# Optimization experiments

Measured on AMD Instinct MI355X. Metric: run time of the kernel, lower is better.

Reference implementation:

```python
import jax, jax.numpy as jnp
import numpy as np

D_MODEL = 1024
NUM_HEADS = 16
DEPTH = D_MODEL // NUM_HEADS
B, S = 2, 2048


def setup_inputs() -> dict:
    key = jax.random.key(0)
    ks = jax.random.split(key, 12)
    scale = 1.0 / np.sqrt(D_MODEL)
    inp = {
        "Q": jax.random.normal(ks[0], (B, S, D_MODEL), jnp.float32),
        "K": jax.random.normal(ks[1], (B, S, D_MODEL), jnp.float32),
        "V": jax.random.normal(ks[2], (B, S, D_MODEL), jnp.float32),
        # causal mask: 1 where attention is disallowed (strictly upper triangular)
        "mask": jnp.triu(jnp.ones((1, 1, S, S), jnp.float32), k=1),
        "Wq": jax.random.normal(ks[3], (D_MODEL, D_MODEL), jnp.float32) * scale,
        "bq": jnp.zeros((D_MODEL,), jnp.float32),
        "Wk": jax.random.normal(ks[4], (D_MODEL, D_MODEL), jnp.float32) * scale,
        "bk": jnp.zeros((D_MODEL,), jnp.float32),
        "Wv": jax.random.normal(ks[5], (D_MODEL, D_MODEL), jnp.float32) * scale,
        "bv": jnp.zeros((D_MODEL,), jnp.float32),
        "Wo": jax.random.normal(ks[6], (D_MODEL, D_MODEL), jnp.float32) * scale,
        "bo": jnp.zeros((D_MODEL,), jnp.float32),
    }
    return inp


def _split_heads(x):
    # [B, S, d_model] -> [B, H, S, depth]
    b, s, _ = x.shape
    return x.reshape(b, s, NUM_HEADS, DEPTH).transpose(0, 2, 1, 3)


def reference(Q, K, V, mask, Wq, bq, Wk, bk, Wv, bv, Wo, bo):
    q = _split_heads(Q @ Wq + bq)  # [B,H,S,depth]
    k = _split_heads(K @ Wk + bk)
    v = _split_heads(V @ Wv + bv)

    scale = 1.0 / jnp.sqrt(jnp.asarray(DEPTH, q.dtype))
    scores = jnp.einsum("bhqd,bhkd->bhqk", q, k) * scale
    scores = scores + mask * (-1e9)
    attn = jax.nn.softmax(scores, axis=-1)  # [B,H,S,S]
    ctx = jnp.einsum("bhqk,bhkd->bhqd", attn, v)

    # combine heads: [B,H,S,depth] -> [B,S,d_model]
    ctx = ctx.transpose(0, 2, 1, 3).reshape(Q.shape[0], -1, D_MODEL)
    out = ctx @ Wo + bo
    return out, attn
```

## Files before the change

kernel.cpp:

```cpp
#include <hip/hip_runtime.h>
#include <hip/hip_bf16.h>
#include <cstdint>
#include <cstddef>


typedef __bf16 bf16x8 __attribute__((ext_vector_type(8)));
typedef float  f32x4  __attribute__((ext_vector_type(4)));
typedef short  short8 __attribute__((ext_vector_type(8)));
typedef unsigned short u16;
typedef unsigned int   u32;

using gas_p = const __attribute__((address_space(1))) void*;
using las_p = __attribute__((address_space(3))) void*;

static __device__ __forceinline__ u16 f2bf(float x) {
    unsigned u = __builtin_bit_cast(unsigned, x);
    u += 0x7FFFu + ((u >> 16) & 1u);
    return (u16)(u >> 16);
}
static __device__ __forceinline__ u32 pk2(float a, float b) {
    return (u32)f2bf(a) | ((u32)f2bf(b) << 16);
}
static __device__ __forceinline__ f32x4 mfma16(bf16x8 a, bf16x8 b, f32x4 c) {
    return __builtin_amdgcn_mfma_f32_16x16x32_bf16(a, b, c, 0, 0, 0);
}
static __device__ __forceinline__ bf16x8 ldb8(const u16* p) {
    return *reinterpret_cast<const bf16x8*>(p);
}

__global__ __launch_bounds__(256) void cvt_bf16_k(const float* __restrict__ Q,
                                                  const float* __restrict__ K,
                                                  const float* __restrict__ V,
                                                  u16* __restrict__ Qb,
                                                  u16* __restrict__ Kb,
                                                  u16* __restrict__ Vb) {
    const int z = blockIdx.y;
    const float* in = (z == 0) ? Q : (z == 1) ? K : V;
    u16* out = (z == 0) ? Qb : (z == 1) ? Kb : Vb;
    size_t i = (size_t)blockIdx.x * 256 + threadIdx.x;
    const float4* p = reinterpret_cast<const float4*>(in) + 2 * i;
    float4 a = p[0], b = p[1];
    short8 r;
    r[0] = (short)f2bf(a.x); r[1] = (short)f2bf(a.y);
    r[2] = (short)f2bf(a.z); r[3] = (short)f2bf(a.w);
    r[4] = (short)f2bf(b.x); r[5] = (short)f2bf(b.y);
    r[6] = (short)f2bf(b.z); r[7] = (short)f2bf(b.w);
    *reinterpret_cast<short8*>(out + 8 * i) = r;
}

__global__ __launch_bounds__(256) void transpose_cvt_k(const float* __restrict__ Wq,
                                                       const float* __restrict__ Wk,
                                                       const float* __restrict__ Wv,
                                                       const float* __restrict__ Wo,
                                                       u16* __restrict__ Wt3,
                                                       u16* __restrict__ Wto) {
    const int z = blockIdx.z;
    const float* in = (z == 0) ? Wq : (z == 1) ? Wk : (z == 2) ? Wv : Wo;
    u16* out = (z < 3) ? (Wt3 + (size_t)z * 1048576) : Wto;
    __shared__ float t[32][33];
    const int tx = threadIdx.x, ty = threadIdx.y;
    const int x  = blockIdx.x * 32 + tx;
    const int y0 = blockIdx.y * 32 + ty;
#pragma unroll
    for (int j = 0; j < 32; j += 8)
        t[ty + j][tx] = in[(size_t)(y0 + j) * 1024 + x];
    __syncthreads();
    const int x2 = blockIdx.y * 32 + tx;
    const int y2 = blockIdx.x * 32 + ty;
#pragma unroll
    for (int j = 0; j < 32; j += 8)
        out[(size_t)(y2 + j) * 1024 + x2] = f2bf(t[tx][ty + j]);
}

__global__ __launch_bounds__(256) void gemm_qkv_k(const u16* __restrict__ Qb,
                                                  const u16* __restrict__ Kb,
                                                  const u16* __restrict__ Vb,
                                                  const u16* __restrict__ Wt3,
                                                  const float* __restrict__ bq,
                                                  const float* __restrict__ bk,
                                                  const float* __restrict__ bv,
                                                  u16* __restrict__ qf,
                                                  u16* __restrict__ kf,
                                                  u16* __restrict__ vtf,
                                                  float* __restrict__ attn) {
    constexpr int Kd = 1024;
    constexpr int S = 2048;
    const int z = blockIdx.z;

    if (z == 3) {
        float* attn_h = attn + (size_t)blockIdx.y * S * S;
        const int bx = blockIdx.x;
        const int ro = threadIdx.x >> 4, cc = threadIdx.x & 15;
        const f32x4 zz = {0.f, 0.f, 0.f, 0.f};
        for (int c = 1; c < 32; ++c) {
            float* base = attn_h + (size_t)(bx * 8 * c) * S + c * 64 + cc * 4;
            const int nrows = 8 * c;
            for (int i = ro; i < nrows; i += 16)
                *reinterpret_cast<f32x4*>(base + (size_t)i * S) = zz;
        }
        return;
    }

    const u16* A  = (z == 0) ? Qb : (z == 1) ? Kb : Vb;
    const u16* Bt = Wt3 + (size_t)z * 1048576;
    const float* bias = (z == 0) ? bq : (z == 1) ? bk : bv;

    __shared__ __align__(16) u16 As[128 * 64];
    __shared__ __align__(16) u16 Bs[128 * 64];
    const int tid = threadIdx.x;
    const int w = tid >> 6, lane = tid & 63;
    const int g = lane >> 4, lr = lane & 15;
    const int wr = w >> 1, wc = w & 1;
    const int bm = blockIdx.y * 128, bn = blockIdx.x * 128;

    f32x4 acc[4][4];
#pragma unroll
    for (int a = 0; a < 4; ++a)
#pragma unroll
        for (int b = 0; b < 4; ++b) acc[a][b] = f32x4{0.f, 0.f, 0.f, 0.f};

    for (int kt = 0; kt < Kd; kt += 64) {
#pragma unroll
        for (int it = 0; it < 4; ++it) {
            const int t2  = it * 256 + tid;
            const int row = t2 >> 3, ch = t2 & 7;
            const int ub  = (it * 256 + w * 64) * 8;
            __builtin_amdgcn_global_load_lds(
                (gas_p)(A + (size_t)(bm + row) * Kd + kt + ch * 8),
                (las_p)(As + ub), 16, 0, 0);
            __builtin_amdgcn_global_load_lds(
                (gas_p)(Bt + (size_t)(bn + row) * Kd + kt + ch * 8),
                (las_p)(Bs + ub), 16, 0, 0);
        }
        __syncthreads();
#pragma unroll
        for (int kk = 0; kk < 2; ++kk) {
            bf16x8 af[4], bfv[4];
#pragma unroll
            for (int mi = 0; mi < 4; ++mi)
                af[mi] = ldb8(As + (wr * 64 + mi * 16 + lr) * 64 + kk * 32 + g * 8);
#pragma unroll
            for (int ni = 0; ni < 4; ++ni)
                bfv[ni] = ldb8(Bs + (wc * 64 + ni * 16 + lr) * 64 + kk * 32 + g * 8);
#pragma unroll
            for (int mi = 0; mi < 4; ++mi)
#pragma unroll
                for (int ni = 0; ni < 4; ++ni)
                    acc[mi][ni] = mfma16(af[mi], bfv[ni], acc[mi][ni]);
        }
        __syncthreads();
    }

#pragma unroll
    for (int ni = 0; ni < 4; ++ni) {
        const int col = bn + wc * 64 + ni * 16 + lr;
        const float bvv = bias[col];
#pragma unroll
        for (int mi = 0; mi < 4; ++mi) {
            const int row0 = bm + wr * 64 + mi * 16 + g * 4;
            f32x4 c = acc[mi][ni];
            if (z == 2) {
                const int b = row0 >> 11, s0 = row0 & 2047;
                const int h = col >> 6,  d = col & 63;
                ushort4 pk;
                pk.x = f2bf(c[0] + bvv); pk.y = f2bf(c[1] + bvv);
                pk.z = f2bf(c[2] + bvv); pk.w = f2bf(c[3] + bvv);
                *reinterpret_cast<ushort4*>(
                    vtf + ((size_t)(b * 16 + h) * 64 + d) * 2048 + s0) = pk;
            } else {
#pragma unroll
                for (int i = 0; i < 4; ++i) {
                    const int row = row0 + i;
                    const int b = row >> 11, s = row & 2047;
                    const int h = col >> 6,  d = col & 63;
                    u16* dst = (z == 0) ? qf : kf;
                    dst[((size_t)(b * 16 + h) * 2048 + s) * 64 + d] =
                        f2bf(c[i] + bvv);
                }
            }
        }
    }
}

__global__ __launch_bounds__(256) void gemm_out_k(const u16* __restrict__ A,
                                                  const u16* __restrict__ Bt,
                                                  const float* __restrict__ bias,
                                                  float* __restrict__ dst) {
    constexpr int Kd = 1024;
    __shared__ __align__(16) u16 As[128 * 64];
    __shared__ __align__(16) u16 Bs[128 * 64];
    const int tid = threadIdx.x;
    const int w = tid >> 6, lane = tid & 63;
    const int g = lane >> 4, lr = lane & 15;
    const int wr = w >> 1, wc = w & 1;
    const int bm = blockIdx.y * 128, bn = blockIdx.x * 128;

    f32x4 acc[4][4];
#pragma unroll
    for (int a = 0; a < 4; ++a)
#pragma unroll
        for (int b = 0; b < 4; ++b) acc[a][b] = f32x4{0.f, 0.f, 0.f, 0.f};

    for (int kt = 0; kt < Kd; kt += 64) {
#pragma unroll
        for (int it = 0; it < 4; ++it) {
            const int t2  = it * 256 + tid;
            const int row = t2 >> 3, ch = t2 & 7;
            const int ub  = (it * 256 + w * 64) * 8;
            __builtin_amdgcn_global_load_lds(
                (gas_p)(A + (size_t)(bm + row) * Kd + kt + ch * 8),
                (las_p)(As + ub), 16, 0, 0);
            __builtin_amdgcn_global_load_lds(
                (gas_p)(Bt + (size_t)(bn + row) * Kd + kt + ch * 8),
                (las_p)(Bs + ub), 16, 0, 0);
        }
        __syncthreads();
#pragma unroll
        for (int kk = 0; kk < 2; ++kk) {
            bf16x8 af[4], bfv[4];
#pragma unroll
            for (int mi = 0; mi < 4; ++mi)
                af[mi] = ldb8(As + (wr * 64 + mi * 16 + lr) * 64 + kk * 32 + g * 8);
#pragma unroll
            for (int ni = 0; ni < 4; ++ni)
                bfv[ni] = ldb8(Bs + (wc * 64 + ni * 16 + lr) * 64 + kk * 32 + g * 8);
#pragma unroll
            for (int mi = 0; mi < 4; ++mi)
#pragma unroll
                for (int ni = 0; ni < 4; ++ni)
                    acc[mi][ni] = mfma16(af[mi], bfv[ni], acc[mi][ni]);
        }
        __syncthreads();
    }

#pragma unroll
    for (int ni = 0; ni < 4; ++ni) {
        const int col = bn + wc * 64 + ni * 16 + lr;
        const float bvv = bias[col];
#pragma unroll
        for (int mi = 0; mi < 4; ++mi) {
            const int row0 = bm + wr * 64 + mi * 16 + g * 4;
            f32x4 c = acc[mi][ni];
#pragma unroll
            for (int i = 0; i < 4; ++i)
                dst[(size_t)(row0 + i) * 1024 + col] = c[i] + bvv;
        }
    }
}

__global__ __launch_bounds__(256) void attn_fused_k(const u16* __restrict__ qbuf,
                                                    const u16* __restrict__ kbuf,
                                                    const u16* __restrict__ vtbuf,
                                                    float* __restrict__ attn,
                                                    u16* __restrict__ ctx) {
    constexpr int S = 2048;
    constexpr float SC2 = 0.125f * 1.44269504088896340736f;
    const int bh = blockIdx.y;
    const int pr = blockIdx.x;
    const int tid = threadIdx.x;
    const int w = tid >> 6, lane = tid & 63, g = lane >> 4, lr = lane & 15;

    const u16* qh = qbuf + (size_t)bh * S * 64;
    const u16* kh = kbuf + (size_t)bh * S * 64;
    const u16* vh = vtbuf + (size_t)bh * 64 * S;
    float* attn_h = attn + (size_t)bh * S * S;

    __shared__ __align__(16) u16 Ks[2][64 * 64];
    __shared__ __align__(16) u16 Vs[2][64 * 64];
    __shared__ __align__(16) u16 P[4][2][16][72];

    const int srow8 = lane >> 3;
    const int scol  = ((lane & 7) ^ srow8) * 8;
    const int swq   = (lr & 7) << 3;
    const int b = bh >> 4, h = bh & 15;

    for (int phase = 0; phase < 2; ++phase) {
        const int j  = phase ? (31 - pr) : pr;
        const int nT = j + 1;
        const int qb = j * 64 + w * 16;
        const int qrow = qb + lr;

        const u16* qp = qh + (size_t)qrow * 64;
        const bf16x8 q0 = ldb8(qp + g * 8);
        const bf16x8 q1 = ldb8(qp + 32 + g * 8);

        float m2 = -1e30f, l = 0.f;
#pragma unroll
        for (int ii = 0; ii < 2; ++ii) {
            const int i = w * 2 + ii, row = i * 8 + srow8;
            __builtin_amdgcn_global_load_lds(
                (gas_p)(kh + (size_t)row * 64 + scol),
                (las_p)(Ks[0] + i * 512), 16, 0, 0);
        }
        __syncthreads();
        for (int t = 0; t < nT; ++t) {
            const int cur = t & 1;
            if (t + 1 < nT) {
#pragma unroll
                for (int ii = 0; ii < 2; ++ii) {
                    const int i = w * 2 + ii;
                    const int row = (t + 1) * 64 + i * 8 + srow8;
                    __builtin_amdgcn_global_load_lds(
                        (gas_p)(kh + (size_t)row * 64 + scol),
                        (las_p)(Ks[cur ^ 1] + i * 512), 16, 0, 0);
                }
                __builtin_amdgcn_sched_barrier(0);
            }
            const int kc = t * 64;
            f32x4 c[4];
#pragma unroll
            for (int n = 0; n < 4; ++n) {
                const u16* kr = Ks[cur] + (n * 16 + lr) * 64;
                f32x4 z4 = {0.f, 0.f, 0.f, 0.f};
                z4   = mfma16(ldb8(kr + ((g * 8) ^ swq)), q0, z4);
                c[n] = mfma16(ldb8(kr + ((32 + g * 8) ^ swq)), q1, z4);
            }
            float xm = -__builtin_inff();
#pragma unroll
            for (int n = 0; n < 4; ++n)
#pragma unroll
                for (int i = 0; i < 4; ++i) {
                    const int kcol = kc + n * 16 + g * 4 + i;
                    const float v = (kcol <= qrow) ? c[n][i] * SC2 : -__builtin_inff();
                    c[n][i] = v;
                    xm = fmaxf(xm, v);
                }
            xm = fmaxf(xm, __shfl_xor(xm, 16));
            xm = fmaxf(xm, __shfl_xor(xm, 32));
            const float mn = fmaxf(m2, xm);
            float sum = 0.f;
#pragma unroll
            for (int n = 0; n < 4; ++n)
#pragma unroll
                for (int i = 0; i < 4; ++i) sum += exp2f(c[n][i] - mn);
            sum += __shfl_xor(sum, 16);
            sum += __shfl_xor(sum, 32);
            l = l * exp2f(m2 - mn) + sum;
            m2 = mn;
            if (t + 1 < nT) {
                asm volatile("s_waitcnt vmcnt(0)" ::: "memory");
                __builtin_amdgcn_s_barrier();
                __builtin_amdgcn_sched_barrier(0);
            }
        }
        const float invl = 1.f / l;

        f32x4 acc[4];
#pragma unroll
        for (int dn = 0; dn < 4; ++dn) acc[dn] = f32x4{0.f, 0.f, 0.f, 0.f};

        __syncthreads();
#pragma unroll
        for (int ii = 0; ii < 2; ++ii) {
            const int i = w * 2 + ii, row = i * 8 + srow8;
            __builtin_amdgcn_global_load_lds(
                (gas_p)(kh + (size_t)row * 64 + scol),
                (las_p)(Ks[0] + i * 512), 16, 0, 0);
            __builtin_amdgcn_global_load_lds(
                (gas_p)(vh + (size_t)row * 2048 + scol),
                (las_p)(Vs[0] + i * 512), 16, 0, 0);
        }
        __syncthreads();
        for (int t = 0; t < nT; ++t) {
            const int cur = t & 1;
            if (t + 1 < nT) {
#pragma unroll
                for (int ii = 0; ii < 2; ++ii) {
                    const int i = w * 2 + ii;
                    const int krow = (t + 1) * 64 + i * 8 + srow8;
                    const int vrow = i * 8 + srow8;
                    __builtin_amdgcn_global_load_lds(
                        (gas_p)(kh + (size_t)krow * 64 + scol),
                        (las_p)(Ks[cur ^ 1] + i * 512), 16, 0, 0);
                    __builtin_amdgcn_global_load_lds(
                        (gas_p)(vh + (size_t)vrow * 2048 + (t + 1) * 64 + scol),
                        (las_p)(Vs[cur ^ 1] + i * 512), 16, 0, 0);
                }
                __builtin_amdgcn_sched_barrier(0);
            }
            const int kc = t * 64;
            f32x4 c[4];
#pragma unroll
            for (int n = 0; n < 4; ++n) {
                const u16* kr = Ks[cur] + (n * 16 + lr) * 64;
                f32x4 z4 = {0.f, 0.f, 0.f, 0.f};
                z4   = mfma16(ldb8(kr + ((g * 8) ^ swq)), q0, z4);
                c[n] = mfma16(ldb8(kr + ((32 + g * 8) ^ swq)), q1, z4);
            }
#pragma unroll
            for (int n = 0; n < 4; ++n) {
                f32x4 pv;
#pragma unroll
                for (int i = 0; i < 4; ++i) {
                    const int kcol = kc + n * 16 + g * 4 + i;
                    pv[i] = (kcol <= qrow) ? exp2f(c[n][i] * SC2 - m2) * invl : 0.f;
                }
                *reinterpret_cast<f32x4*>(attn_h + (size_t)qrow * S + kc + n * 16 + g * 4) = pv;
                uint2 pr2;
                pr2.x = pk2(pv[0], pv[1]);
                pr2.y = pk2(pv[2], pv[3]);
                *reinterpret_cast<uint2*>(&P[w][t & 1][lr][n * 16 + g * 4]) = pr2;
            }
            asm volatile("s_waitcnt lgkmcnt(0)" ::: "memory");
            __builtin_amdgcn_sched_barrier(0);
#pragma unroll
            for (int kk = 0; kk < 2; ++kk) {
                const bf16x8 pa = ldb8(&P[w][t & 1][lr][kk * 32 + g * 8]);
#pragma unroll
                for (int dn = 0; dn < 4; ++dn) {
                    const u16* vr = Vs[cur] + (dn * 16 + lr) * 64;
                    acc[dn] = mfma16(pa, ldb8(vr + ((kk * 32 + g * 8) ^ swq)), acc[dn]);
                }
            }
            if (t + 1 < nT) {
                asm volatile("s_waitcnt vmcnt(4)" ::: "memory");
                __builtin_amdgcn_s_barrier();
                __builtin_amdgcn_sched_barrier(0);
            }
        }

#pragma unroll
        for (int dn = 0; dn < 4; ++dn)
#pragma unroll
            for (int i = 0; i < 4; ++i) {
                const size_t row = (size_t)b * S + qb + g * 4 + i;
                ctx[row * 1024 + h * 64 + dn * 16 + lr] = f2bf(acc[dn][i]);
            }
        __syncthreads();
    }
}

extern "C" void kernel_launch(void* const* d_in, const int* in_sizes, int n_in,
                              void* d_out, int out_size, void* d_ws, size_t ws_size,
                              hipStream_t stream) {
    (void)in_sizes; (void)n_in; (void)out_size; (void)ws_size;

    const float* Q  = (const float*)d_in[0];
    const float* K  = (const float*)d_in[1];
    const float* V  = (const float*)d_in[2];
    const float* Wq = (const float*)d_in[4];
    const float* bq = (const float*)d_in[5];
    const float* Wk = (const float*)d_in[6];
    const float* bk = (const float*)d_in[7];
    const float* Wv = (const float*)d_in[8];
    const float* bv = (const float*)d_in[9];
    const float* Wo = (const float*)d_in[10];
    const float* bo = (const float*)d_in[11];

    char* ws = (char*)d_ws;
    u16* Qb  = (u16*)(ws);
    u16* Kb  = (u16*)(ws + ((size_t)8  << 20));
    u16* Vb  = (u16*)(ws + ((size_t)16 << 20));
    u16* Wt3 = (u16*)(ws + ((size_t)24 << 20));
    u16* Wto = (u16*)(ws + ((size_t)30 << 20));
    u16* qf  = (u16*)(ws + ((size_t)32 << 20));
    u16* kf  = (u16*)(ws + ((size_t)40 << 20));
    u16* vtf = (u16*)(ws + ((size_t)48 << 20));
    u16* ctx = (u16*)(ws + ((size_t)56 << 20));

    float* out  = (float*)d_out;
    float* attn = out + (size_t)4096 * 1024;

    cvt_bf16_k<<<dim3(2048, 3), 256, 0, stream>>>(Q, K, V, Qb, Kb, Vb);

    transpose_cvt_k<<<dim3(32, 32, 4), dim3(32, 8), 0, stream>>>(Wq, Wk, Wv, Wo, Wt3, Wto);

    gemm_qkv_k<<<dim3(8, 32, 4), 256, 0, stream>>>(Qb, Kb, Vb, Wt3, bq, bk, bv,
                                                   qf, kf, vtf, attn);

    attn_fused_k<<<dim3(16, 32), 256, 0, stream>>>(qf, kf, vtf, attn, ctx);

    gemm_out_k<<<dim3(8, 32), 256, 0, stream>>>(ctx, Wto, bo, out);
}
```

Measured before the change: 291.6 us.

## Fuse fp32-to-bf16 input conversion into QKV GEMM, triple-buffer attention loads, nontemporal stores

Removes the separate fp32->bf16 conversion kernel for Q/K/V. The QKV GEMM now loads fp32 activations into registers, converts them, and writes bf16 to LDS itself. The attention kernel moves from double- to triple-buffered K/V tiles with a two-ahead prefetch, and drops the double buffering of the P scratch. Stores of attention probabilities, zero-fill and GEMM outputs become nontemporal. Together these save a kernel launch and a round trip through the intermediate buffer, and give more latency hiding. The cost is that the GEMM A loads are now synchronous register loads with a full vmcnt(0) wait, which may stall it. It also re-reads fp32 A once per N tile (8x) instead of bf16.

```diff
diff --git a/kernel.cpp b/kernel.cpp
--- a/kernel.cpp
+++ b/kernel.cpp
@@ -6,7 +6,6 @@
 
 typedef __bf16 bf16x8 __attribute__((ext_vector_type(8)));
 typedef float  f32x4  __attribute__((ext_vector_type(4)));
-typedef short  short8 __attribute__((ext_vector_type(8)));
 typedef unsigned short u16;
 typedef unsigned int   u32;
 
@@ -26,26 +25,6 @@
 }
 static __device__ __forceinline__ bf16x8 ldb8(const u16* p) {
     return *reinterpret_cast<const bf16x8*>(p);
-}
-
-__global__ __launch_bounds__(256) void cvt_bf16_k(const float* __restrict__ Q,
-                                                  const float* __restrict__ K,
-                                                  const float* __restrict__ V,
-                                                  u16* __restrict__ Qb,
-                                                  u16* __restrict__ Kb,
-                                                  u16* __restrict__ Vb) {
-    const int z = blockIdx.y;
-    const float* in = (z == 0) ? Q : (z == 1) ? K : V;
-    u16* out = (z == 0) ? Qb : (z == 1) ? Kb : Vb;
-    size_t i = (size_t)blockIdx.x * 256 + threadIdx.x;
-    const float4* p = reinterpret_cast<const float4*>(in) + 2 * i;
-    float4 a = p[0], b = p[1];
-    short8 r;
-    r[0] = (short)f2bf(a.x); r[1] = (short)f2bf(a.y);
-    r[2] = (short)f2bf(a.z); r[3] = (short)f2bf(a.w);
-    r[4] = (short)f2bf(b.x); r[5] = (short)f2bf(b.y);
-    r[6] = (short)f2bf(b.z); r[7] = (short)f2bf(b.w);
-    *reinterpret_cast<short8*>(out + 8 * i) = r;
 }
 
 __global__ __launch_bounds__(256) void transpose_cvt_k(const float* __restrict__ Wq,
@@ -72,9 +51,9 @@
         out[(size_t)(y2 + j) * 1024 + x2] = f2bf(t[tx][ty + j]);
 }
 
-__global__ __launch_bounds__(256) void gemm_qkv_k(const u16* __restrict__ Qb,
-                                                  const u16* __restrict__ Kb,
-                                                  const u16* __restrict__ Vb,
+__global__ __launch_bounds__(256) void gemm_qkv_k(const float* __restrict__ Qf,
+                                                  const float* __restrict__ Kf,
+                                                  const float* __restrict__ Vf,
                                                   const u16* __restrict__ Wt3,
                                                   const float* __restrict__ bq,
                                                   const float* __restrict__ bk,
@@ -96,12 +75,12 @@
             float* base = attn_h + (size_t)(bx * 8 * c) * S + c * 64 + cc * 4;
             const int nrows = 8 * c;
             for (int i = ro; i < nrows; i += 16)
-                *reinterpret_cast<f32x4*>(base + (size_t)i * S) = zz;
+                __builtin_nontemporal_store(zz, reinterpret_cast<f32x4*>(base + (size_t)i * S));
         }
         return;
     }
 
-    const u16* A  = (z == 0) ? Qb : (z == 1) ? Kb : Vb;
+    const float* Af = (z == 0) ? Qf : (z == 1) ? Kf : Vf;
     const u16* Bt = Wt3 + (size_t)z * 1048576;
     const float* bias = (z == 0) ? bq : (z == 1) ? bk : bv;
 
@@ -119,18 +98,35 @@
 #pragma unroll
         for (int b = 0; b < 4; ++b) acc[a][b] = f32x4{0.f, 0.f, 0.f, 0.f};
 
+    const int arow = tid >> 3;
+    const int ach  = tid & 7;
+
     for (int kt = 0; kt < Kd; kt += 64) {
+        float4 av[8];
+#pragma unroll
+        for (int it = 0; it < 4; ++it) {
+            const float* src = Af + (size_t)(bm + it * 32 + arow) * Kd + kt + ach * 8;
+            av[it * 2]     = *reinterpret_cast<const float4*>(src);
+            av[it * 2 + 1] = *reinterpret_cast<const float4*>(src + 4);
+        }
 #pragma unroll
         for (int it = 0; it < 4; ++it) {
             const int t2  = it * 256 + tid;
             const int row = t2 >> 3, ch = t2 & 7;
             const int ub  = (it * 256 + w * 64) * 8;
             __builtin_amdgcn_global_load_lds(
-                (gas_p)(A + (size_t)(bm + row) * Kd + kt + ch * 8),
-                (las_p)(As + ub), 16, 0, 0);
-            __builtin_amdgcn_global_load_lds(
                 (gas_p)(Bt + (size_t)(bn + row) * Kd + kt + ch * 8),
                 (las_p)(Bs + ub), 16, 0, 0);
+        }
+        asm volatile("s_waitcnt vmcnt(0)" ::: "memory");
+#pragma unroll
+        for (int it = 0; it < 4; ++it) {
+            uint4 pk;
+            pk.x = pk2(av[it * 2].x, av[it * 2].y);
+            pk.y = pk2(av[it * 2].z, av[it * 2].w);
+            pk.z = pk2(av[it * 2 + 1].x, av[it * 2 + 1].y);
+            pk.w = pk2(av[it * 2 + 1].z, av[it * 2 + 1].w);
+            *reinterpret_cast<uint4*>(As + (it * 32 + arow) * 64 + ach * 8) = pk;
         }
         __syncthreads();
 #pragma unroll
@@ -243,7 +239,8 @@
             f32x4 c = acc[mi][ni];
 #pragma unroll
             for (int i = 0; i < 4; ++i)
-                dst[(size_t)(row0 + i) * 1024 + col] = c[i] + bvv;
+                __builtin_nontemporal_store(c[i] + bvv,
+                                            dst + (size_t)(row0 + i) * 1024 + col);
         }
     }
 }
@@ -265,9 +262,9 @@
     const u16* vh = vtbuf + (size_t)bh * 64 * S;
     float* attn_h = attn + (size_t)bh * S * S;
 
-    __shared__ __align__(16) u16 Ks[2][64 * 64];
-    __shared__ __align__(16) u16 Vs[2][64 * 64];
-    __shared__ __align__(16) u16 P[4][2][16][72];
+    __shared__ __align__(16) u16 Ks[3][64 * 64];
+    __shared__ __align__(16) u16 Vs[3][64 * 64];
+    __shared__ __align__(16) u16 P[4][16][72];
 
     const int srow8 = lane >> 3;
     const int scol  = ((lane & 7) ^ srow8) * 8;
@@ -284,26 +281,36 @@
         const bf16x8 q0 = ldb8(qp + g * 8);
         const bf16x8 q1 = ldb8(qp + 32 + g * 8);
 
+        const int i0 = w * 2, i1 = w * 2 + 1;
+        const int r0 = i0 * 8 + srow8, r1 = i1 * 8 + srow8;
+
         float m2 = -1e30f, l = 0.f;
-#pragma unroll
-        for (int ii = 0; ii < 2; ++ii) {
-            const int i = w * 2 + ii, row = i * 8 + srow8;
-            __builtin_amdgcn_global_load_lds(
-                (gas_p)(kh + (size_t)row * 64 + scol),
-                (las_p)(Ks[0] + i * 512), 16, 0, 0);
-        }
-        __syncthreads();
+        __builtin_amdgcn_global_load_lds((gas_p)(kh + (size_t)r0 * 64 + scol),
+                                         (las_p)(Ks[0] + i0 * 512), 16, 0, 0);
+        __builtin_amdgcn_global_load_lds((gas_p)(kh + (size_t)r1 * 64 + scol),
+                                         (las_p)(Ks[0] + i1 * 512), 16, 0, 0);
+        if (nT > 1) {
+            __builtin_amdgcn_global_load_lds((gas_p)(kh + (size_t)(64 + r0) * 64 + scol),
+                                             (las_p)(Ks[1] + i0 * 512), 16, 0, 0);
+            __builtin_amdgcn_global_load_lds((gas_p)(kh + (size_t)(64 + r1) * 64 + scol),
+                                             (las_p)(Ks[1] + i1 * 512), 16, 0, 0);
+            asm volatile("s_waitcnt vmcnt(2)" ::: "memory");
+        } else {
+            asm volatile("s_waitcnt vmcnt(0)" ::: "memory");
+        }
+        __builtin_amdgcn_s_barrier();
+        __builtin_amdgcn_sched_barrier(0);
+
+        int cur = 0, stg = 2;
         for (int t = 0; t < nT; ++t) {
-            const int cur = t & 1;
-            if (t + 1 < nT) {
-#pragma unroll
-                for (int ii = 0; ii < 2; ++ii) {
-                    const int i = w * 2 + ii;
-                    const int row = (t + 1) * 64 + i * 8 + srow8;
-                    __builtin_amdgcn_global_load_lds(
-                        (gas_p)(kh + (size_t)row * 64 + scol),
-                        (las_p)(Ks[cur ^ 1] + i * 512), 16, 0, 0);
-                }
+            if (t + 2 < nT) {
+                const int kr0 = (t + 2) * 64;
+                __builtin_amdgcn_global_load_lds(
+                    (gas_p)(kh + (size_t)(kr0 + r0) * 64 + scol),
+                    (las_p)(Ks[stg] + i0 * 512), 16, 0, 0);
+                __builtin_amdgcn_global_load_lds(
+                    (gas_p)(kh + (size_t)(kr0 + r1) * 64 + scol),
+                    (las_p)(Ks[stg] + i1 * 512), 16, 0, 0);
                 __builtin_amdgcn_sched_barrier(0);
             }
             const int kc = t * 64;
@@ -338,10 +345,16 @@
             l = l * exp2f(m2 - mn) + sum;
             m2 = mn;
             if (t + 1 < nT) {
-                asm volatile("s_waitcnt vmcnt(0)" ::: "memory");
+                if (t + 2 < nT) {
+                    asm volatile("s_waitcnt vmcnt(2)" ::: "memory");
+                } else {
+                    asm volatile("s_waitcnt vmcnt(0)" ::: "memory");
+                }
                 __builtin_amdgcn_s_barrier();
                 __builtin_amdgcn_sched_barrier(0);
             }
+            cur = (cur == 2) ? 0 : cur + 1;
+            stg = (stg == 2) ? 0 : stg + 1;
         }
         const float invl = 1.f / l;
 
@@ -350,32 +363,46 @@
         for (int dn = 0; dn < 4; ++dn) acc[dn] = f32x4{0.f, 0.f, 0.f, 0.f};
 
         __syncthreads();
-#pragma unroll
-        for (int ii = 0; ii < 2; ++ii) {
-            const int i = w * 2 + ii, row = i * 8 + srow8;
-            __builtin_amdgcn_global_load_lds(
-                (gas_p)(kh + (size_t)row * 64 + scol),
-                (las_p)(Ks[0] + i * 512), 16, 0, 0);
-            __builtin_amdgcn_global_load_lds(
-                (gas_p)(vh + (size_t)row * 2048 + scol),
-                (las_p)(Vs[0] + i * 512), 16, 0, 0);
-        }
-        __syncthreads();
+        __builtin_amdgcn_global_load_lds((gas_p)(kh + (size_t)r0 * 64 + scol),
+                                         (las_p)(Ks[0] + i0 * 512), 16, 0, 0);
+        __builtin_amdgcn_global_load_lds((gas_p)(kh + (size_t)r1 * 64 + scol),
+                                         (las_p)(Ks[0] + i1 * 512), 16, 0, 0);
+        __builtin_amdgcn_global_load_lds((gas_p)(vh + (size_t)r0 * 2048 + scol),
+                                         (las_p)(Vs[0] + i0 * 512), 16, 0, 0);
+        __builtin_amdgcn_global_load_lds((gas_p)(vh + (size_t)r1 * 2048 + scol),
+                                         (las_p)(Vs[0] + i1 * 512), 16, 0, 0);
+        if (nT > 1) {
+            __builtin_amdgcn_global_load_lds((gas_p)(kh + (size_t)(64 + r0) * 64 + scol),
+                                             (las_p)(Ks[1] + i0 * 512), 16, 0, 0);
+            __builtin_amdgcn_global_load_lds((gas_p)(kh + (size_t)(64 + r1) * 64 + scol),
+                                             (las_p)(Ks[1] + i1 * 512), 16, 0, 0);
+            __builtin_amdgcn_global_load_lds((gas_p)(vh + (size_t)r0 * 2048 + 64 + scol),
+                                             (las_p)(Vs[1] + i0 * 512), 16, 0, 0);
+            __builtin_amdgcn_global_load_lds((gas_p)(vh + (size_t)r1 * 2048 + 64 + scol),
+                                             (las_p)(Vs[1] + i1 * 512), 16, 0, 0);
+            asm volatile("s_waitcnt vmcnt(4)" ::: "memory");
+        } else {
+            asm volatile("s_waitcnt vmcnt(0)" ::: "memory");
+        }
+        __builtin_amdgcn_s_barrier();
+        __builtin_amdgcn_sched_barrier(0);
+
+        cur = 0; stg = 2;
         for (int t = 0; t < nT; ++t) {
-            const int cur = t & 1;
-            if (t + 1 < nT) {
-#pragma unroll
-                for (int ii = 0; ii < 2; ++ii) {
-                    const int i = w * 2 + ii;
-                    const int krow = (t + 1) * 64 + i * 8 + srow8;
-                    const int vrow = i * 8 + srow8;
-                    __builtin_amdgcn_global_load_lds(
-                        (gas_p)(kh + (size_t)krow * 64 + scol),
-                        (las_p)(Ks[cur ^ 1] + i * 512), 16, 0, 0);
-                    __builtin_amdgcn_global_load_lds(
-                        (gas_p)(vh + (size_t)vrow * 2048 + (t + 1) * 64 + scol),
-                        (las_p)(Vs[cur ^ 1] + i * 512), 16, 0, 0);
-                }
+            if (t + 2 < nT) {
+                const int kr0 = (t + 2) * 64;
+                __builtin_amdgcn_global_load_lds(
+                    (gas_p)(kh + (size_t)(kr0 + r0) * 64 + scol),
+                    (las_p)(Ks[stg] + i0 * 512), 16, 0, 0);
+                __builtin_amdgcn_global_load_lds(
+                    (gas_p)(kh + (size_t)(kr0 + r1) * 64 + scol),
+                    (las_p)(Ks[stg] + i1 * 512), 16, 0, 0);
+                __builtin_amdgcn_global_load_lds(
+                    (gas_p)(vh + (size_t)r0 * 2048 + kr0 + scol),
+                    (las_p)(Vs[stg] + i0 * 512), 16, 0, 0);
+                __builtin_amdgcn_global_load_lds(
+                    (gas_p)(vh + (size_t)r1 * 2048 + kr0 + scol),
+                    (las_p)(Vs[stg] + i1 * 512), 16, 0, 0);
                 __builtin_amdgcn_sched_barrier(0);
             }
             const int kc = t * 64;
@@ -395,17 +422,18 @@
                     const int kcol = kc + n * 16 + g * 4 + i;
                     pv[i] = (kcol <= qrow) ? exp2f(c[n][i] * SC2 - m2) * invl : 0.f;
                 }
-                *reinterpret_cast<f32x4*>(attn_h + (size_t)qrow * S + kc + n * 16 + g * 4) = pv;
+                __builtin_nontemporal_store(
+                    pv, reinterpret_cast<f32x4*>(attn_h + (size_t)qrow * S + kc + n * 16 + g * 4));
                 uint2 pr2;
                 pr2.x = pk2(pv[0], pv[1]);
                 pr2.y = pk2(pv[2], pv[3]);
-                *reinterpret_cast<uint2*>(&P[w][t & 1][lr][n * 16 + g * 4]) = pr2;
+                *reinterpret_cast<uint2*>(&P[w][lr][n * 16 + g * 4]) = pr2;
             }
             asm volatile("s_waitcnt lgkmcnt(0)" ::: "memory");
             __builtin_amdgcn_sched_barrier(0);
 #pragma unroll
             for (int kk = 0; kk < 2; ++kk) {
-                const bf16x8 pa = ldb8(&P[w][t & 1][lr][kk * 32 + g * 8]);
+                const bf16x8 pa = ldb8(&P[w][lr][kk * 32 + g * 8]);
 #pragma unroll
                 for (int dn = 0; dn < 4; ++dn) {
                     const u16* vr = Vs[cur] + (dn * 16 + lr) * 64;
@@ -413,10 +441,16 @@
                 }
             }
             if (t + 1 < nT) {
-                asm volatile("s_waitcnt vmcnt(4)" ::: "memory");
+                if (t + 2 < nT) {
+                    asm volatile("s_waitcnt vmcnt(8)" ::: "memory");
+                } else {
+                    asm volatile("s_waitcnt vmcnt(4)" ::: "memory");
+                }
                 __builtin_amdgcn_s_barrier();
                 __builtin_amdgcn_sched_barrier(0);
             }
+            cur = (cur == 2) ? 0 : cur + 1;
+            stg = (stg == 2) ? 0 : stg + 1;
         }
 
 #pragma unroll
@@ -448,24 +482,19 @@
     const float* bo = (const float*)d_in[11];
 
     char* ws = (char*)d_ws;
-    u16* Qb  = (u16*)(ws);
-    u16* Kb  = (u16*)(ws + ((size_t)8  << 20));
-    u16* Vb  = (u16*)(ws + ((size_t)16 << 20));
-    u16* Wt3 = (u16*)(ws + ((size_t)24 << 20));
-    u16* Wto = (u16*)(ws + ((size_t)30 << 20));
-    u16* qf  = (u16*)(ws + ((size_t)32 << 20));
-    u16* kf  = (u16*)(ws + ((size_t)40 << 20));
-    u16* vtf = (u16*)(ws + ((size_t)48 << 20));
-    u16* ctx = (u16*)(ws + ((size_t)56 << 20));
+    u16* Wt3 = (u16*)(ws);
+    u16* Wto = (u16*)(ws + ((size_t)6  << 20));
+    u16* qf  = (u16*)(ws + ((size_t)8  << 20));
+    u16* kf  = (u16*)(ws + ((size_t)16 << 20));
+    u16* vtf = (u16*)(ws + ((size_t)24 << 20));
+    u16* ctx = (u16*)(ws + ((size_t)32 << 20));
 
     float* out  = (float*)d_out;
     float* attn = out + (size_t)4096 * 1024;
 
-    cvt_bf16_k<<<dim3(2048, 3), 256, 0, stream>>>(Q, K, V, Qb, Kb, Vb);
-
     transpose_cvt_k<<<dim3(32, 32, 4), dim3(32, 8), 0, stream>>>(Wq, Wk, Wv, Wo, Wt3, Wto);
 
-    gemm_qkv_k<<<dim3(8, 32, 4), 256, 0, stream>>>(Qb, Kb, Vb, Wt3, bq, bk, bv,
+    gemm_qkv_k<<<dim3(8, 32, 4), 256, 0, stream>>>(Q, K, V, Wt3, bq, bk, bv,
                                                    qf, kf, vtf, attn);
 
     attn_fused_k<<<dim3(16, 32), 256, 0, stream>>>(qf, kf, vtf, attn, ctx);
```

Result: slower. 321.6 us (+10.3%).
